# Performance work log

Measured on AMD Instinct MI355X. Metric: run time of the kernel, lower is better.

The kernel has to match this reference:

```python
import jax, jax.numpy as jnp
import numpy as np

B, N = 4, 512
NZ = 95
BOX = 25.0                      # Angstrom box for random coords
CUTOFF = 15.0
SMOOTH_ON = 12.0                # cutoff * (1 - 0.2)
SMOOTH_OFF = 15.0
A1, A2, S6, S8 = 0.4145, 4.8593, 1.0, 1.2177
K1, K3 = 16.0, 4.0              # standard DFT-D3 CN / gaussian-weight constants
BOHR = 1.8897261258369282       # Angstrom -> Bohr
H2EV = 27.211386245988          # Hartree -> eV


def setup_inputs() -> dict:
    key = jax.random.key(0)
    k = jax.random.split(key, 6)
    coord = jax.random.uniform(k[0], (B, N, 3), jnp.float32) * BOX
    numbers = jax.random.randint(k[1], (B, N), 0, 86).astype(jnp.int64)
    rcov = jax.random.uniform(k[2], (NZ,), jnp.float32) * 2.0 + 1.0      # Bohr
    r4r2 = jax.random.uniform(k[3], (NZ,), jnp.float32) * 3.0 + 2.0      # a.u.
    c6ab = jax.random.uniform(k[4], (NZ, NZ, 5, 5), jnp.float32) * 20.0 + 1.0
    cn_ref = jax.random.uniform(k[5], (NZ, NZ, 5, 5), jnp.float32) * 4.0
    return dict(coord=coord, numbers=numbers, rcov=rcov, r4r2=r4r2,
                c6ab=c6ab, cn_ref=cn_ref)


def _d3_energy(coord, rcov, r4r2, c6ab, cn_ref, numbers):
    z = numbers
    # pairwise distances [B,N,N] (Angstrom), self-pairs masked
    diff = coord[:, :, None, :] - coord[:, None, :, :]
    r2 = (diff * diff).sum(-1)
    eye = jnp.eye(N, dtype=bool)[None]
    r2_safe = jnp.where(eye, 1.0, r2)
    r_ang = jnp.sqrt(r2_safe)
    pair_mask = (~eye) & (r_ang <= CUTOFF)
    r = r_ang * BOHR  # Bohr

    # coordination numbers: CN_i = sum_j 1/(1+exp(-k1*(rcov_ij/r - 1)))
    rc = rcov[z]                                   # [B,N]
    rco = rc[:, :, None] + rc[:, None, :]          # [B,N,N]
    cn_pair = jnp.where(pair_mask,
                        1.0 / (1.0 + jnp.exp(-K1 * (rco / r - 1.0))), 0.0)
    cn = cn_pair.sum(-1)                           # [B,N]

    # C6 interpolation over 5x5 reference-CN grid (gather-heavy)
    zi = z[:, :, None]   # [B,N,1]
    zj = z[:, None, :]   # [B,1,N]
    c6_ref = c6ab[zi, zj]                               # [B,N,N,5,5]
    cni_ref = cn_ref[zi, zj]                            # ref CN of atom i
    cnj_ref = jnp.swapaxes(cn_ref[zj, zi], -1, -2)      # ref CN of atom j
    dcn_i = cn[:, :, None, None, None] - cni_ref
    dcn_j = cn[:, None, :, None, None] - cnj_ref
    w = jnp.where(c6_ref > 0.0,
                  jnp.exp(-K3 * (dcn_i * dcn_i + dcn_j * dcn_j)), 0.0)
    wsum = w.sum((-1, -2))
    c6 = (c6_ref * w).sum((-1, -2)) / (wsum + 1e-20)    # [B,N,N]

    # C8 and BJ damping radius
    rr = r4r2[z]
    r4r2ij = rr[:, :, None] * rr[:, None, :]
    c8 = 3.0 * c6 * r4r2ij
    r0 = jnp.sqrt(3.0 * r4r2ij)     # sqrt(C8/C6)
    f = A1 * r0 + A2

    r6 = r2_safe * BOHR * BOHR
    r6 = r6 * r6 * r6               # r^6 in Bohr
    r8 = r6 * r * r
    e_pair = S6 * c6 / (r6 + f ** 6) + S8 * c8 / (r8 + f ** 8)

    # cutoff smoothing (smoothstep from SMOOTH_ON to SMOOTH_OFF, in Angstrom)
    x = jnp.clip((r_ang - SMOOTH_ON) / (SMOOTH_OFF - SMOOTH_ON), 0.0, 1.0)
    sw = 1.0 - x * x * (3.0 - 2.0 * x)
    e_pair = jnp.where(pair_mask, e_pair * sw, 0.0)

    # each pair counted twice in the dense matrix -> 0.5 factor; Hartree->eV
    return -0.5 * e_pair.sum((1, 2)) * H2EV   # [B]


def reference(coord, numbers, rcov, r4r2, c6ab, cn_ref):
    return _d3_energy(coord, rcov, r4r2, c6ab, cn_ref, numbers)
```

## Files before the change

### kernel.cpp

```cpp
#include <hip/hip_runtime.h>

#define NA   512
#define NB   4
#define NZT  95

#define FUSED_ELEMS (NZT * NZT * 25)
#define FUSED_BYTES (FUSED_ELEMS * 16)
#define FUSE_BLOCKS ((FUSED_ELEMS + 255) / 256)

#define SORT_OFF (((FUSED_BYTES + 63) / 64) * 64)
#define ARR_B    (NB * NA * 4)
#define EBLOCKS  (NB * NA / 2)

__global__ void __launch_bounds__(256) prep_kernel(
    const float* __restrict__ coord,
    const int*   __restrict__ numbers,
    const float* __restrict__ rcov,
    const float* __restrict__ r4r2,
    const float* __restrict__ c6ab,
    const float* __restrict__ cn_ref,
    float4*      __restrict__ fused,
    float*       __restrict__ xs,
    float*       __restrict__ ys,
    float*       __restrict__ zs,
    float*       __restrict__ rcs,
    float*       __restrict__ rrs,
    int*         __restrict__ zsp)
{
    const int blk = blockIdx.x;
    if (blk < NB) {
        const int b = blk;
        __shared__ int hist[NZT];
        __shared__ int offs[NZT];
        for (int t = threadIdx.x; t < NZT; t += 256) hist[t] = 0;
        __syncthreads();

        const int i0 = threadIdx.x;
        const int i1 = threadIdx.x + 256;
        const int z0 = numbers[b * NA + i0];
        const int z1 = numbers[b * NA + i1];
        atomicAdd(&hist[z0], 1);
        atomicAdd(&hist[z1], 1);
        __syncthreads();
        if (threadIdx.x == 0) {
            int s = 0;
            for (int k = 0; k < NZT; ++k) { offs[k] = s; s += hist[k]; }
        }
        __syncthreads();

        const float* cb = coord + (size_t)b * NA * 3;
        const int base = b * NA;

        const int p0 = base + atomicAdd(&offs[z0], 1);
        xs[p0]  = cb[3 * i0 + 0];
        ys[p0]  = cb[3 * i0 + 1];
        zs[p0]  = cb[3 * i0 + 2];
        rcs[p0] = rcov[z0];
        rrs[p0] = r4r2[z0];
        zsp[p0] = z0;

        const int p1 = base + atomicAdd(&offs[z1], 1);
        xs[p1]  = cb[3 * i1 + 0];
        ys[p1]  = cb[3 * i1 + 1];
        zs[p1]  = cb[3 * i1 + 2];
        rcs[p1] = rcov[z1];
        rrs[p1] = r4r2[z1];
        zsp[p1] = z1;
        return;
    }

    const int idx = (blk - NB) * 256 + threadIdx.x;
    if (idx >= FUSED_ELEMS) return;
    const int pair = idx / 25;
    const int k    = idx - pair * 25;
    const int a    = k / 5;
    const int b2   = k - a * 5;
    const int zi   = pair / NZT;
    const int zj   = pair - zi * NZT;
    const int pt   = zj * NZT + zi;
    const int kt   = b2 * 5 + a;

    const float c6s = c6ab[(size_t)pair * 25 + k] + c6ab[(size_t)pt * 25 + kt];
    const float ci  = cn_ref[(size_t)pair * 25 + k];
    const float cj  = cn_ref[(size_t)pt * 25 + kt];
    fused[idx] = make_float4(c6s, ci, cj, 0.0f);
}

__global__ void __launch_bounds__(256) cn_kernel(
    const float* __restrict__ xs,
    const float* __restrict__ ys,
    const float* __restrict__ zs,
    const float* __restrict__ rcs,
    float*       __restrict__ cn)
{
    const int bi   = blockIdx.x;
    const int b    = bi >> 9;
    const int i    = bi & (NA - 1);
    const int base = b * NA;

    const float xi  = xs[base + i];
    const float yi  = ys[base + i];
    const float zi  = zs[base + i];
    const float rci = rcs[base + i];

    float acc = 0.0f;
    #pragma unroll
    for (int t = 0; t < 2; ++t) {
        const int j = threadIdx.x + t * 256;
        if (j == i) continue;
        const float dx = xi - xs[base + j];
        const float dy = yi - ys[base + j];
        const float dz = zi - zs[base + j];
        const float r2 = dx * dx + dy * dy + dz * dz;
        const float r_ang = sqrtf(r2);
        if (r_ang <= 15.0f) {
            const float rb  = r_ang * 1.8897261258369282f;
            const float rco = rci + rcs[base + j];
            acc += 1.0f / (1.0f + __expf(-16.0f * (rco / rb - 1.0f)));
        }
    }
    #pragma unroll
    for (int off = 32; off > 0; off >>= 1)
        acc += __shfl_down(acc, off, 64);

    __shared__ float red[4];
    const int wave = threadIdx.x >> 6;
    if ((threadIdx.x & 63) == 0) red[wave] = acc;
    __syncthreads();
    if (threadIdx.x == 0) cn[bi] = red[0] + red[1] + red[2] + red[3];
}

__global__ void __launch_bounds__(256) energy_kernel(
    const float*  __restrict__ xs,
    const float*  __restrict__ ys,
    const float*  __restrict__ zs,
    const float*  __restrict__ rrs,
    const int*    __restrict__ zsp,
    const float4* __restrict__ fused,
    const float*  __restrict__ cn,
    float*        __restrict__ partials)
{
    const int blk  = blockIdx.x;
    const int b    = blk >> 8;
    const int ih   = blk & 255;
    const int iA   = ih;
    const int iB   = NA - 1 - ih;
    const int cntA = NA - 1 - iA;
    const int base = b * NA;

    const float xA = xs[base + iA],  xB = xs[base + iB];
    const float yA = ys[base + iA],  yB = ys[base + iB];
    const float zA = zs[base + iA],  zB = zs[base + iB];
    const float cA = cn[base + iA],  cB = cn[base + iB];
    const float rA = rrs[base + iA], rB = rrs[base + iB];
    const int   sA = zsp[base + iA], sB = zsp[base + iB];

    float e = 0.0f;
    #pragma unroll
    for (int t = 0; t < 2; ++t) {
        const int u = threadIdx.x + t * 256;
        if (u >= NA - 1) continue;
        const bool inA = (u < cntA);
        const int  j   = inA ? (iA + 1 + u) : (u + 1);

        const float xi  = inA ? xA : xB;
        const float yi  = inA ? yA : yB;
        const float zci = inA ? zA : zB;

        const float dx = xi - xs[base + j];
        const float dy = yi - ys[base + j];
        const float dz = zci - zs[base + j];
        const float r2 = dx * dx + dy * dy + dz * dz;
        const float r_ang = sqrtf(r2);
        if (r_ang <= 15.0f) {
            const float cni = inA ? cA : cB;
            const float rri = inA ? rA : rB;
            const int   zi  = inA ? sA : sB;
            const int   zj  = zsp[base + j];
            const float cnj = cn[base + j];

            const float4* tp = fused + ((size_t)zi * NZT + zj) * 25;

            float wsum = 0.0f, c6w = 0.0f;
            #pragma unroll
            for (int k = 0; k < 25; ++k) {
                const float4 tv = tp[k];
                const float di = cni - tv.y;
                const float dj = cnj - tv.z;
                float s = di * di;
                s = fmaf(dj, dj, s);
                const float w = __expf(-4.0f * s);
                wsum += w;
                c6w  = fmaf(tv.x, w, c6w);
            }
            const float c6 = c6w / (wsum + 1e-20f);

            const float rrij = rri * rrs[base + j];
            const float c8f  = 3.0f * rrij;
            const float r0   = sqrtf(3.0f * rrij);
            const float f    = 0.4145f * r0 + 4.8593f;

            const float B2  = 1.8897261258369282f * 1.8897261258369282f;
            const float r2b = r2 * B2;
            const float r6  = r2b * r2b * r2b;
            const float r8  = r6 * r2b;
            const float f2  = f * f;
            const float f6  = f2 * f2 * f2;
            const float f8  = f6 * f2;

            float ep = c6 / (r6 + f6) + 1.2177f * (c6 * c8f) / (r8 + f8);

            float x = (r_ang - 12.0f) * (1.0f / 3.0f);
            x = fminf(fmaxf(x, 0.0f), 1.0f);
            const float sw = 1.0f - x * x * (3.0f - 2.0f * x);
            e = fmaf(ep, sw, e);
        }
    }

    #pragma unroll
    for (int off = 32; off > 0; off >>= 1)
        e += __shfl_down(e, off, 64);

    __shared__ float red[4];
    const int wave = threadIdx.x >> 6;
    if ((threadIdx.x & 63) == 0) red[wave] = e;
    __syncthreads();
    if (threadIdx.x == 0)
        partials[blk] = red[0] + red[1] + red[2] + red[3];
}

__global__ void __launch_bounds__(256) reduce_kernel(
    const float* __restrict__ partials,
    float*       __restrict__ out)
{
    const int b = blockIdx.x;
    const int P = EBLOCKS / NB;
    float s = partials[b * P + threadIdx.x];

    #pragma unroll
    for (int off = 32; off > 0; off >>= 1)
        s += __shfl_down(s, off, 64);

    __shared__ float red[4];
    const int wave = threadIdx.x >> 6;
    if ((threadIdx.x & 63) == 0) red[wave] = s;
    __syncthreads();
    if (threadIdx.x == 0) {
        const float tot = red[0] + red[1] + red[2] + red[3];
        out[b] = tot * (-0.5f * 27.211386245988f);
    }
}

extern "C" void kernel_launch(void* const* d_in, const int* in_sizes, int n_in,
                              void* d_out, int out_size, void* d_ws, size_t ws_size,
                              hipStream_t stream) {
    const float* coord   = (const float*)d_in[0];
    const int*   numbers = (const int*)  d_in[1];
    const float* rcov    = (const float*)d_in[2];
    const float* r4r2    = (const float*)d_in[3];
    const float* c6ab    = (const float*)d_in[4];
    const float* cn_ref  = (const float*)d_in[5];
    float* out = (float*)d_out;

    char* ws = (char*)d_ws;
    float4* fused = (float4*)ws;
    float*  xs   = (float*)(ws + SORT_OFF + 0 * ARR_B);
    float*  ys   = (float*)(ws + SORT_OFF + 1 * ARR_B);
    float*  zs   = (float*)(ws + SORT_OFF + 2 * ARR_B);
    float*  rcs  = (float*)(ws + SORT_OFF + 3 * ARR_B);
    float*  rrs  = (float*)(ws + SORT_OFF + 4 * ARR_B);
    int*    zsp  = (int*)  (ws + SORT_OFF + 5 * ARR_B);
    float*  cn   = (float*)(ws + SORT_OFF + 6 * ARR_B);
    float*  part = (float*)(ws + SORT_OFF + 7 * ARR_B);

    prep_kernel<<<NB + FUSE_BLOCKS, 256, 0, stream>>>(
        coord, numbers, rcov, r4r2, c6ab, cn_ref,
        fused, xs, ys, zs, rcs, rrs, zsp);

    cn_kernel<<<NB * NA, 256, 0, stream>>>(xs, ys, zs, rcs, cn);

    energy_kernel<<<EBLOCKS, 256, 0, stream>>>(xs, ys, zs, rrs, zsp,
                                               fused, cn, part);

    reduce_kernel<<<NB, 256, 0, stream>>>(part, out);
}
```

Measured before the change: 83.97 us.

## Merge CN pass into prep kernel and fold final reduction into energy kernel

The coordination-number computation now runs in extra blocks of the prep kernel, reading unsorted coordinates directly, and a permutation array maps sorted indices back to the unsorted CN values. The separate reduce kernel is removed: energy blocks atomically accumulate per-batch sums and the last block, found with an atomic counter, writes the output. This cuts the launch count from four to two and drops a dependency barrier. In exchange it adds an indirect gather through perm in the hot energy loop, uses strided AoS coordinate reads in the CN pass, and makes the float summation order nondeterministic.

```diff
diff --git a/kernel.cpp b/kernel.cpp
--- a/kernel.cpp
+++ b/kernel.cpp
@@ -7,12 +7,13 @@
 #define FUSED_ELEMS (NZT * NZT * 25)
 #define FUSED_BYTES (FUSED_ELEMS * 16)
 #define FUSE_BLOCKS ((FUSED_ELEMS + 255) / 256)
+#define CN_BLOCKS   (NB * NA)
+#define EBLOCKS     (NB * NA / 2)
 
 #define SORT_OFF (((FUSED_BYTES + 63) / 64) * 64)
 #define ARR_B    (NB * NA * 4)
-#define EBLOCKS  (NB * NA / 2)
-
-__global__ void __launch_bounds__(256) prep_kernel(
+
+__global__ void __launch_bounds__(256) prep_all_kernel(
     const float* __restrict__ coord,
     const int*   __restrict__ numbers,
     const float* __restrict__ rcov,
@@ -23,11 +24,15 @@
     float*       __restrict__ xs,
     float*       __restrict__ ys,
     float*       __restrict__ zs,
-    float*       __restrict__ rcs,
     float*       __restrict__ rrs,
-    int*         __restrict__ zsp)
+    int*         __restrict__ zsp,
+    int*         __restrict__ perm,
+    float*       __restrict__ cn_u,
+    float*       __restrict__ acc,
+    unsigned*    __restrict__ counter)
 {
     const int blk = blockIdx.x;
+
     if (blk < NB) {
         const int b = blk;
         __shared__ int hist[NZT];
@@ -55,79 +60,79 @@
         xs[p0]  = cb[3 * i0 + 0];
         ys[p0]  = cb[3 * i0 + 1];
         zs[p0]  = cb[3 * i0 + 2];
-        rcs[p0] = rcov[z0];
         rrs[p0] = r4r2[z0];
         zsp[p0] = z0;
+        perm[p0] = i0;
 
         const int p1 = base + atomicAdd(&offs[z1], 1);
         xs[p1]  = cb[3 * i1 + 0];
         ys[p1]  = cb[3 * i1 + 1];
         zs[p1]  = cb[3 * i1 + 2];
-        rcs[p1] = rcov[z1];
         rrs[p1] = r4r2[z1];
         zsp[p1] = z1;
+        perm[p1] = i1;
         return;
     }
 
-    const int idx = (blk - NB) * 256 + threadIdx.x;
-    if (idx >= FUSED_ELEMS) return;
-    const int pair = idx / 25;
-    const int k    = idx - pair * 25;
-    const int a    = k / 5;
-    const int b2   = k - a * 5;
-    const int zi   = pair / NZT;
-    const int zj   = pair - zi * NZT;
-    const int pt   = zj * NZT + zi;
-    const int kt   = b2 * 5 + a;
-
-    const float c6s = c6ab[(size_t)pair * 25 + k] + c6ab[(size_t)pt * 25 + kt];
-    const float ci  = cn_ref[(size_t)pair * 25 + k];
-    const float cj  = cn_ref[(size_t)pt * 25 + kt];
-    fused[idx] = make_float4(c6s, ci, cj, 0.0f);
-}
-
-__global__ void __launch_bounds__(256) cn_kernel(
-    const float* __restrict__ xs,
-    const float* __restrict__ ys,
-    const float* __restrict__ zs,
-    const float* __restrict__ rcs,
-    float*       __restrict__ cn)
-{
-    const int bi   = blockIdx.x;
+    if (blk < NB + FUSE_BLOCKS) {
+        if (blk == NB && threadIdx.x < NB + 1) {
+            if (threadIdx.x < NB) acc[threadIdx.x * 16] = 0.0f;
+            else                  *counter = 0u;
+        }
+        const int idx = (blk - NB) * 256 + threadIdx.x;
+        if (idx >= FUSED_ELEMS) return;
+        const int pair = idx / 25;
+        const int k    = idx - pair * 25;
+        const int a    = k / 5;
+        const int b2   = k - a * 5;
+        const int zi   = pair / NZT;
+        const int zj   = pair - zi * NZT;
+        const int pt   = zj * NZT + zi;
+        const int kt   = b2 * 5 + a;
+
+        const float c6s = c6ab[(size_t)pair * 25 + k] + c6ab[(size_t)pt * 25 + kt];
+        const float ci  = cn_ref[(size_t)pair * 25 + k];
+        const float cj  = cn_ref[(size_t)pt * 25 + kt];
+        fused[idx] = make_float4(c6s, ci, cj, 0.0f);
+        return;
+    }
+
+    const int bi   = blk - NB - FUSE_BLOCKS;
     const int b    = bi >> 9;
     const int i    = bi & (NA - 1);
-    const int base = b * NA;
-
-    const float xi  = xs[base + i];
-    const float yi  = ys[base + i];
-    const float zi  = zs[base + i];
-    const float rci = rcs[base + i];
-
-    float acc = 0.0f;
+    const float* cb = coord   + (size_t)b * NA * 3;
+    const int*   nb = numbers + (size_t)b * NA;
+
+    const float xi  = cb[3 * i + 0];
+    const float yi  = cb[3 * i + 1];
+    const float zi  = cb[3 * i + 2];
+    const float rci = rcov[nb[i]];
+
+    float acc_cn = 0.0f;
     #pragma unroll
     for (int t = 0; t < 2; ++t) {
         const int j = threadIdx.x + t * 256;
         if (j == i) continue;
-        const float dx = xi - xs[base + j];
-        const float dy = yi - ys[base + j];
-        const float dz = zi - zs[base + j];
+        const float dx = xi - cb[3 * j + 0];
+        const float dy = yi - cb[3 * j + 1];
+        const float dz = zi - cb[3 * j + 2];
         const float r2 = dx * dx + dy * dy + dz * dz;
         const float r_ang = sqrtf(r2);
         if (r_ang <= 15.0f) {
             const float rb  = r_ang * 1.8897261258369282f;
-            const float rco = rci + rcs[base + j];
-            acc += 1.0f / (1.0f + __expf(-16.0f * (rco / rb - 1.0f)));
+            const float rco = rci + rcov[nb[j]];
+            acc_cn += 1.0f / (1.0f + __expf(-16.0f * (rco / rb - 1.0f)));
         }
     }
     #pragma unroll
     for (int off = 32; off > 0; off >>= 1)
-        acc += __shfl_down(acc, off, 64);
+        acc_cn += __shfl_down(acc_cn, off, 64);
 
     __shared__ float red[4];
     const int wave = threadIdx.x >> 6;
-    if ((threadIdx.x & 63) == 0) red[wave] = acc;
+    if ((threadIdx.x & 63) == 0) red[wave] = acc_cn;
     __syncthreads();
-    if (threadIdx.x == 0) cn[bi] = red[0] + red[1] + red[2] + red[3];
+    if (threadIdx.x == 0) cn_u[bi] = red[0] + red[1] + red[2] + red[3];
 }
 
 __global__ void __launch_bounds__(256) energy_kernel(
@@ -136,9 +141,12 @@
     const float*  __restrict__ zs,
     const float*  __restrict__ rrs,
     const int*    __restrict__ zsp,
+    const int*    __restrict__ perm,
     const float4* __restrict__ fused,
-    const float*  __restrict__ cn,
-    float*        __restrict__ partials)
+    const float*  __restrict__ cn_u,
+    float*        __restrict__ acc,
+    unsigned*     __restrict__ counter,
+    float*        __restrict__ out)
 {
     const int blk  = blockIdx.x;
     const int b    = blk >> 8;
@@ -151,7 +159,8 @@
     const float xA = xs[base + iA],  xB = xs[base + iB];
     const float yA = ys[base + iA],  yB = ys[base + iB];
     const float zA = zs[base + iA],  zB = zs[base + iB];
-    const float cA = cn[base + iA],  cB = cn[base + iB];
+    const float cA = cn_u[base + perm[base + iA]];
+    const float cB = cn_u[base + perm[base + iB]];
     const float rA = rrs[base + iA], rB = rrs[base + iB];
     const int   sA = zsp[base + iA], sB = zsp[base + iB];
 
@@ -177,7 +186,7 @@
             const float rri = inA ? rA : rB;
             const int   zi  = inA ? sA : sB;
             const int   zj  = zsp[base + j];
-            const float cnj = cn[base + j];
+            const float cnj = cn_u[base + perm[base + j]];
 
             const float4* tp = fused + ((size_t)zi * NZT + zj) * 25;
 
@@ -225,29 +234,19 @@
     const int wave = threadIdx.x >> 6;
     if ((threadIdx.x & 63) == 0) red[wave] = e;
     __syncthreads();
-    if (threadIdx.x == 0)
-        partials[blk] = red[0] + red[1] + red[2] + red[3];
-}
-
-__global__ void __launch_bounds__(256) reduce_kernel(
-    const float* __restrict__ partials,
-    float*       __restrict__ out)
-{
-    const int b = blockIdx.x;
-    const int P = EBLOCKS / NB;
-    float s = partials[b * P + threadIdx.x];
-
-    #pragma unroll
-    for (int off = 32; off > 0; off >>= 1)
-        s += __shfl_down(s, off, 64);
-
-    __shared__ float red[4];
-    const int wave = threadIdx.x >> 6;
-    if ((threadIdx.x & 63) == 0) red[wave] = s;
-    __syncthreads();
+
     if (threadIdx.x == 0) {
-        const float tot = red[0] + red[1] + red[2] + red[3];
-        out[b] = tot * (-0.5f * 27.211386245988f);
+        const float s = red[0] + red[1] + red[2] + red[3];
+        atomicAdd(&acc[b * 16], s);
+        __threadfence();
+        const unsigned old = atomicAdd(counter, 1u);
+        if (old == EBLOCKS - 1) {
+            #pragma unroll
+            for (int q = 0; q < NB; ++q) {
+                const float v = atomicAdd(&acc[q * 16], 0.0f);
+                out[q] = v * (-0.5f * 27.211386245988f);
+            }
+        }
     }
 }
 
@@ -263,24 +262,21 @@
     float* out = (float*)d_out;
 
     char* ws = (char*)d_ws;
-    float4* fused = (float4*)ws;
-    float*  xs   = (float*)(ws + SORT_OFF + 0 * ARR_B);
-    float*  ys   = (float*)(ws + SORT_OFF + 1 * ARR_B);
-    float*  zs   = (float*)(ws + SORT_OFF + 2 * ARR_B);
-    float*  rcs  = (float*)(ws + SORT_OFF + 3 * ARR_B);
-    float*  rrs  = (float*)(ws + SORT_OFF + 4 * ARR_B);
-    int*    zsp  = (int*)  (ws + SORT_OFF + 5 * ARR_B);
-    float*  cn   = (float*)(ws + SORT_OFF + 6 * ARR_B);
-    float*  part = (float*)(ws + SORT_OFF + 7 * ARR_B);
-
-    prep_kernel<<<NB + FUSE_BLOCKS, 256, 0, stream>>>(
+    float4*   fused   = (float4*)ws;
+    float*    xs      = (float*)(ws + SORT_OFF + 0 * ARR_B);
+    float*    ys      = (float*)(ws + SORT_OFF + 1 * ARR_B);
+    float*    zs      = (float*)(ws + SORT_OFF + 2 * ARR_B);
+    float*    rrs     = (float*)(ws + SORT_OFF + 3 * ARR_B);
+    int*      zsp     = (int*)  (ws + SORT_OFF + 4 * ARR_B);
+    int*      perm    = (int*)  (ws + SORT_OFF + 5 * ARR_B);
+    float*    cn_u    = (float*)(ws + SORT_OFF + 6 * ARR_B);
+    float*    acc     = (float*)(ws + SORT_OFF + 7 * ARR_B);
+    unsigned* counter = (unsigned*)(ws + SORT_OFF + 7 * ARR_B + 512);
+
+    prep_all_kernel<<<NB + FUSE_BLOCKS + CN_BLOCKS, 256, 0, stream>>>(
         coord, numbers, rcov, r4r2, c6ab, cn_ref,
-        fused, xs, ys, zs, rcs, rrs, zsp);
-
-    cn_kernel<<<NB * NA, 256, 0, stream>>>(xs, ys, zs, rcs, cn);
-
-    energy_kernel<<<EBLOCKS, 256, 0, stream>>>(xs, ys, zs, rrs, zsp,
-                                               fused, cn, part);
-
-    reduce_kernel<<<NB, 256, 0, stream>>>(part, out);
+        fused, xs, ys, zs, rrs, zsp, perm, cn_u, acc, counter);
+
+    energy_kernel<<<EBLOCKS, 256, 0, stream>>>(
+        xs, ys, zs, rrs, zsp, perm, fused, cn_u, acc, counter, out);
 }
```

Result: slower. 99.67 us (+18.7%).
